# Kernel optimization log

Hardware: AMD Instinct MI355X
Metric: run time of the kernel (lower is better)

## Reference

```python
import jax, jax.numpy as jnp
import numpy as np

EPS_LN = 1e-5
EPS_ATTN = 1e-8
NUM_ITER = 3

B, N, DIN = 64, 4096, 256
K, D, H = 8, 256, 512


def layer_norm(x, g, b):
    m = jnp.mean(x, axis=-1, keepdims=True)
    v = jnp.mean((x - m) ** 2, axis=-1, keepdims=True)
    return (x - m) * jax.lax.rsqrt(v + EPS_LN) * g + b


def gru_cell(x, h, W_ih, b_ih, W_hh, b_hh):
    # torch GRUCell: gates ordered (reset, update, new)
    gi = x @ W_ih.T + b_ih  # [BK, 3D]
    gh = h @ W_hh.T + b_hh
    ir, iz, inn = jnp.split(gi, 3, axis=-1)
    hr, hz, hn = jnp.split(gh, 3, axis=-1)
    r = jax.nn.sigmoid(ir + hr)
    z = jax.nn.sigmoid(iz + hz)
    n = jnp.tanh(inn + r * hn)
    return (1.0 - z) * n + z * h


def setup_inputs() -> dict:
    key = jax.random.key(0)
    ks = jax.random.split(key, 16)
    s = 1.0 / np.sqrt(D)
    si = 1.0 / np.sqrt(DIN)
    inp = {
        'inputs': jax.random.normal(ks[0], (B, N, DIN), jnp.float32),
        'noise': jax.random.normal(ks[1], (B, K, D), jnp.float32),
        'slot_mu': jax.random.normal(ks[2], (1, 1, D), jnp.float32),
        'slot_log_sigma': jnp.zeros((1, 1, D), jnp.float32),
        'Wq': jax.random.uniform(ks[3], (D, D), jnp.float32, -s, s),
        'bq': jnp.zeros((D,), jnp.float32),
        'Wk': jax.random.uniform(ks[4], (D, DIN), jnp.float32, -si, si),
        'bk': jnp.zeros((D,), jnp.float32),
        'Wv': jax.random.uniform(ks[5], (D, DIN), jnp.float32, -si, si),
        'bv': jnp.zeros((D,), jnp.float32),
        'W_ih': jax.random.uniform(ks[6], (3 * D, D), jnp.float32, -s, s),
        'b_ih': jnp.zeros((3 * D,), jnp.float32),
        'W_hh': jax.random.uniform(ks[7], (3 * D, D), jnp.float32, -s, s),
        'b_hh': jnp.zeros((3 * D,), jnp.float32),
        'ln_in_g': jnp.ones((DIN,), jnp.float32), 'ln_in_b': jnp.zeros((DIN,), jnp.float32),
        'ln_s_g': jnp.ones((D,), jnp.float32), 'ln_s_b': jnp.zeros((D,), jnp.float32),
        'ln_ff_g': jnp.ones((D,), jnp.float32), 'ln_ff_b': jnp.zeros((D,), jnp.float32),
        'W1': jax.random.uniform(ks[8], (H, D), jnp.float32, -s, s),
        'b1': jnp.zeros((H,), jnp.float32),
        'W2': jax.random.uniform(ks[9], (D, H), jnp.float32, -1.0 / np.sqrt(H), 1.0 / np.sqrt(H)),
        'b2': jnp.zeros((D,), jnp.float32),
    }
    return inp


def reference(inputs, noise, slot_mu, slot_log_sigma, Wq, bq, Wk, bk, Wv, bv,
              W_ih, b_ih, W_hh, b_hh, ln_in_g, ln_in_b, ln_s_g, ln_s_b,
              ln_ff_g, ln_ff_b, W1, b1, W2, b2):
    scale = D ** -0.5
    slots = slot_mu + jnp.exp(slot_log_sigma) * noise  # [B,K,D]
    x = layer_norm(inputs, ln_in_g, ln_in_b)
    k = x @ Wk.T + bk  # [B,N,D]
    v = x @ Wv.T + bv  # [B,N,D]
    attn = None
    for _ in range(NUM_ITER):
        slots_prev = slots
        sn = layer_norm(slots, ln_s_g, ln_s_b)
        q = sn @ Wq.T + bq  # [B,K,D]
        dots = jnp.einsum('bkd,bnd->bkn', q, k) * scale
        attn = jax.nn.softmax(dots, axis=1)  # softmax over slots
        attn_norm = attn / (jnp.sum(attn, axis=-1, keepdims=True) + EPS_ATTN)
        updates = jnp.einsum('bkn,bnd->bkd', attn_norm, v)
        h = gru_cell(updates.reshape(-1, D), slots_prev.reshape(-1, D),
                     W_ih, b_ih, W_hh, b_hh).reshape(slots.shape)
        ff = layer_norm(h, ln_ff_g, ln_ff_b)
        slots = h + (jax.nn.relu(ff @ W1.T + b1) @ W2.T + b2)
    return slots, attn
```

## Files before the change

### kernel.cpp

```cpp
#include <hip/hip_runtime.h>
#include <hip/hip_bf16.h>
#include <math.h>

typedef __bf16 bf16x8 __attribute__((ext_vector_type(8)));
typedef float f32x4 __attribute__((ext_vector_type(4)));

#define DEV static __device__ __forceinline__

DEV unsigned short f2b(float f){
  unsigned int u = __float_as_uint(f);
  u += 0x7fffu + ((u>>16)&1u);
  return (unsigned short)(u>>16);
}
DEV float b2f(unsigned short h){ return __uint_as_float(((unsigned int)h)<<16); }
DEV unsigned int pck(float a, float b){
  return (unsigned int)f2b(a) | ((unsigned int)f2b(b)<<16);
}
DEV f32x4 mfma16(bf16x8 a, bf16x8 b, f32x4 c){
  return __builtin_amdgcn_mfma_f32_16x16x32_bf16(a,b,c,0,0,0);
}
DEV float sigm(float x){ return 1.f/(1.f+expf(-x)); }
#define RDLANE(v, l) __uint_as_float(__builtin_amdgcn_readlane(__float_as_uint(v), (l)))

__global__ __launch_bounds__(256) void k_slots_init(
    const float* __restrict__ noise, const float* __restrict__ mu,
    const float* __restrict__ ls, float* __restrict__ sf,
    unsigned short* __restrict__ sb){
  int i = blockIdx.x*256 + threadIdx.x;
  int d = i & 255;
  float val = mu[d] + expf(ls[d]) * noise[i];
  sf[i] = val; sb[i] = f2b(val);
}

__global__ __launch_bounds__(256) void k_prep_b16(
    const float* __restrict__ Whh, const float* __restrict__ W1,
    const float* __restrict__ W2,
    unsigned short* __restrict__ Whhb, unsigned short* __restrict__ W1b,
    unsigned short* __restrict__ W2b){
  int i = blockIdx.x*256 + threadIdx.x;
  if (i < 196608) Whhb[i] = f2b(Whh[i]);
  else if (i < 327680) W1b[i-196608] = f2b(W1[i-196608]);
  else if (i < 458752) W2b[i-327680] = f2b(W2[i-327680]);
}

__global__ __launch_bounds__(256) void k_pre1(
    const float* __restrict__ Wq, const float* __restrict__ Wk,
    const float* __restrict__ bq, const float* __restrict__ bk,
    unsigned short* __restrict__ WcT, float* __restrict__ bc,
    float* __restrict__ wqbk, float* __restrict__ cbk){
  int c = blockIdx.x, d = threadIdx.x;
  float acc = 0.f;
  for (int e=0;e<256;e++)
    acc += Wq[e*256+d] * Wk[e*256+c];
  WcT[c*256+d] = f2b(acc);
  __shared__ float red[256];
  red[d] = bq[d] * Wk[d*256+c];
  __syncthreads();
  for (int s2=128;s2>0;s2>>=1){ if (d<s2) red[d]+=red[d+s2]; __syncthreads(); }
  if (d==0) bc[c] = red[0];
  if (blockIdx.x==0){
    float a2=0.f;
    for (int e=0;e<256;e++) a2 += Wq[e*256+d]*bk[e];
    wqbk[d] = a2;
    __syncthreads();
    red[d] = bq[d]*bk[d];
    __syncthreads();
    for (int s2=128;s2>0;s2>>=1){ if (d<s2) red[d]+=red[d+s2]; __syncthreads(); }
    if (d==0) cbk[0] = red[0];
  }
}

__global__ __launch_bounds__(256) void k_pre2(
    const float* __restrict__ W_ih, const float* __restrict__ Wv,
    const float* __restrict__ bv, const float* __restrict__ b_ih,
    unsigned short* __restrict__ WvihT, float* __restrict__ bvih){
  int j = blockIdx.x, c = threadIdx.x;
  float acc=0.f;
  for (int d=0; d<256; d++)
    acc += W_ih[j*256+d] * Wv[d*256+c];
  WvihT[j*256+c] = f2b(acc);
  __shared__ float red[256];
  red[c] = bv[c] * W_ih[j*256+c];
  __syncthreads();
  for (int s2=128;s2>0;s2>>=1){ if (c<s2) red[c]+=red[c+s2]; __syncthreads(); }
  if (c==0) bvih[j] = red[0] + b_ih[j];
}

__global__ __launch_bounds__(256) void k_slot_q(
    const float* __restrict__ sf, const float* __restrict__ g,
    const float* __restrict__ be,
    const unsigned short* __restrict__ WcT, const float* __restrict__ bc,
    const float* __restrict__ wqbk, const float* __restrict__ cbk,
    unsigned short* __restrict__ qp, float* __restrict__ dotbias,
    float* __restrict__ attn_sum){
  __shared__ __align__(16) unsigned short sn[16][264];
  int b = blockIdx.x, t = threadIdx.x;
  if (t < 8) attn_sum[b*8+t] = 0.f;
  if (t < 8) dotbias[b*16+8+t] = 0.f;
  int r = t>>5, j = t&31;
  const float* pr = sf + (b*8+r)*256 + j*8;
  float v[8]; float s=0.f;
  #pragma unroll
  for (int i=0;i<8;i++){ v[i]=pr[i]; s+=v[i]; }
  s += __shfl_xor(s,1); s+=__shfl_xor(s,2); s+=__shfl_xor(s,4);
  s += __shfl_xor(s,8); s+=__shfl_xor(s,16);
  float m = s*(1.f/256.f);
  float vs=0.f;
  #pragma unroll
  for (int i=0;i<8;i++){ float d = v[i]-m; vs += d*d; }
  vs += __shfl_xor(vs,1); vs+=__shfl_xor(vs,2); vs+=__shfl_xor(vs,4);
  vs += __shfl_xor(vs,8); vs+=__shfl_xor(vs,16);
  float rstd = rsqrtf(vs*(1.f/256.f) + 1e-5f);
  float dp = 0.f;
  #pragma unroll
  for (int i=0;i<8;i++){
    int d = j*8+i;
    float snv = (v[i]-m)*rstd*g[d] + be[d];
    sn[r][d] = f2b(snv);
    dp += snv * wqbk[d];
  }
  dp += __shfl_xor(dp,1); dp+=__shfl_xor(dp,2); dp+=__shfl_xor(dp,4);
  dp += __shfl_xor(dp,8); dp+=__shfl_xor(dp,16);
  if (j==0) dotbias[b*16+r] = dp + cbk[0];
  for (int rr=8; rr<16; ++rr){ sn[rr][t]=0; if (t<8) sn[rr][256+t]=0; }
  __syncthreads();
  int lane = t&63, wv = t>>6, l16 = lane&15, quad = lane>>4;
  #pragma unroll
  for (int nt=0; nt<4; ++nt){
    int col = (wv*4+nt)*16 + l16;
    f32x4 acc = {0.f,0.f,0.f,0.f};
    #pragma unroll
    for (int kk=0;kk<8;kk++){
      int kd = kk*32 + quad*8;
      bf16x8 a = *(const bf16x8*)&sn[l16][kd];
      bf16x8 bb = *(const bf16x8*)(WcT + col*256 + kd);
      acc = mfma16(a,bb,acc);
    }
    float bcv = bc[col];
    #pragma unroll
    for (int ri=0;ri<4;ri++){
      int rw = quad*4+ri;
      qp[(b*16+rw)*256 + col] = f2b(acc[ri] + bcv);
    }
  }
}

__global__ __launch_bounds__(256) void k_iter0(
    const float* __restrict__ in, const float* __restrict__ g,
    const float* __restrict__ be, const unsigned short* __restrict__ qp,
    const float* __restrict__ dotbias, float* __restrict__ attn_sum,
    float* __restrict__ upart, unsigned short* __restrict__ xc_w){
  __shared__ __align__(16) unsigned short xt[64][264];
  int t = threadIdx.x;
  int b = blockIdx.x >> 4, sp = blockIdx.x & 15;
  int lane=t&63, wv=t>>6, l16=lane&15, quad=lane>>4;
  bf16x8 aq[8];
  #pragma unroll
  for (int kk=0;kk<8;kk++)
    aq[kk] = *(const bf16x8*)(qp + ((size_t)(b*16+l16))*256 + kk*32+quad*8);
  float db[4];
  #pragma unroll
  for (int ri=0;ri<4;ri++) db[ri] = dotbias[b*16 + quad*4 + ri];
  float acc[8][4];
  #pragma unroll
  for (int k2=0;k2<8;k2++){ acc[k2][0]=0;acc[k2][1]=0;acc[k2][2]=0;acc[k2][3]=0; }
  float rbs[4] = {0.f,0.f,0.f,0.f};
  int rl = t>>3, j = t&7;
  for (int tile=0; tile<4; ++tile){
    int n0 = sp*256 + tile*64;
    __syncthreads();
    #pragma unroll
    for (int p=0;p<2;p++){
      int row = p*32 + rl;
      const float* pr = in + ((size_t)(b*4096 + n0 + row))*256 + j*32;
      float v[32]; float s=0.f;
      #pragma unroll
      for (int c=0;c<8;c++) *(float4*)(v+c*4) = *(const float4*)(pr + c*4);
      #pragma unroll
      for (int i=0;i<32;i++) s += v[i];
      s += __shfl_xor(s,1); s+=__shfl_xor(s,2); s+=__shfl_xor(s,4);
      float m = s*(1.f/256.f);
      float vs=0.f;
      #pragma unroll
      for (int i=0;i<32;i++){ float d=v[i]-m; vs+=d*d; }
      vs+=__shfl_xor(vs,1); vs+=__shfl_xor(vs,2); vs+=__shfl_xor(vs,4);
      float rstd = rsqrtf(vs*(1.f/256.f)+1e-5f);
      #pragma unroll
      for (int c=0;c<4;c++){
        float o[8];
        #pragma unroll
        for (int q=0;q<8;q++){
          int d = j*32 + c*8 + q;
          o[q] = (v[c*8+q]-m)*rstd*g[d] + be[d];
        }
        uint4 w4;
        w4.x=pck(o[0],o[1]); w4.y=pck(o[2],o[3]);
        w4.z=pck(o[4],o[5]); w4.w=pck(o[6],o[7]);
        *(uint4*)&xt[row][j*32 + c*8] = w4;
        *(uint4*)(xc_w + ((size_t)(b*4096 + n0 + row))*256 + j*32 + c*8) = w4;
      }
    }
    __syncthreads();
    f32x4 dacc = {0.f,0.f,0.f,0.f};
    #pragma unroll
    for (int kk=0;kk<8;kk++){
      int kd = kk*32 + quad*8;
      bf16x8 bb = *(const bf16x8*)&xt[wv*16 + l16][kd];
      dacc = mfma16(aq[kk],bb,dacc);
    }
    const float scale = 0.0625f;
    float val[4];
    #pragma unroll
    for (int ri=0;ri<4;ri++) val[ri] = (dacc[ri] + db[ri]) * scale;
    float mx = fmaxf(fmaxf(val[0],val[1]), fmaxf(val[2],val[3]));
    mx = fmaxf(mx, __shfl_xor(mx,16));
    float e[4], s4=0.f;
    #pragma unroll
    for (int ri=0;ri<4;ri++){ e[ri] = expf(val[ri]-mx); s4 += e[ri]; }
    float s8 = s4 + __shfl_xor(s4,16);
    float inv = 1.f/s8;
    float av[4];
    #pragma unroll
    for (int ri=0;ri<4;ri++) av[ri] = e[ri]*inv;
    if (quad < 2){
      #pragma unroll
      for (int ri=0;ri<4;ri++){
        float ss = av[ri];
        ss += __shfl_xor(ss,1); ss+=__shfl_xor(ss,2);
        ss += __shfl_xor(ss,4); ss+=__shfl_xor(ss,8);
        if (l16==0) rbs[ri] += ss;
      }
    }
    #pragma unroll
    for (int nl=0; nl<16; ++nl){
      int n = wv*16 + nl;
      float xv0 = b2f(xt[n][lane]);
      float xv1 = b2f(xt[n][64+lane]);
      float xv2 = b2f(xt[n][128+lane]);
      float xv3 = b2f(xt[n][192+lane]);
      #pragma unroll
      for (int ri=0;ri<4;ri++){
        float alo = RDLANE(av[ri], nl);
        float ahi = RDLANE(av[ri], nl+16);
        acc[ri][0]   += alo*xv0; acc[ri][1]   += alo*xv1;
        acc[ri][2]   += alo*xv2; acc[ri][3]   += alo*xv3;
        acc[4+ri][0] += ahi*xv0; acc[4+ri][1] += ahi*xv1;
        acc[4+ri][2] += ahi*xv2; acc[4+ri][3] += ahi*xv3;
      }
    }
  }
  __syncthreads();
  float* ured = (float*)&xt[0][0];
  #pragma unroll
  for (int k2=0;k2<8;k2++)
    #pragma unroll
    for (int cc=0;cc<4;cc++)
      ured[(wv*8+k2)*256 + cc*64 + lane] = acc[k2][cc];
  __syncthreads();
  float* o = upart + (size_t)sp*131072 + ((size_t)b*8)*256 + t;
  #pragma unroll
  for (int k2=0;k2<8;k2++){
    float s = ured[k2*256+t] + ured[(8+k2)*256+t]
            + ured[(16+k2)*256+t] + ured[(24+k2)*256+t];
    o[(size_t)k2*256] = s;
  }
  if (quad < 2 && l16 == 0){
    #pragma unroll
    for (int ri=0;ri<4;ri++)
      atomicAdd(&attn_sum[b*8 + quad*4 + ri], rbs[ri]);
  }
}

__global__ __launch_bounds__(256) void k_iter(
    const unsigned short* __restrict__ xc,
    const unsigned short* __restrict__ qp,
    const float* __restrict__ dotbias, float* __restrict__ attn_sum,
    float* __restrict__ upart, float* __restrict__ attn_out){
  __shared__ __align__(16) unsigned short xt[64][264];
  int t = threadIdx.x;
  int b = blockIdx.x >> 4, sp = blockIdx.x & 15;
  int lane=t&63, wv=t>>6, l16=lane&15, quad=lane>>4;
  bf16x8 aq[8];
  #pragma unroll
  for (int kk=0;kk<8;kk++)
    aq[kk] = *(const bf16x8*)(qp + ((size_t)(b*16+l16))*256 + kk*32+quad*8);
  float db[4];
  #pragma unroll
  for (int ri=0;ri<4;ri++) db[ri] = dotbias[b*16 + quad*4 + ri];
  float acc[8][4];
  #pragma unroll
  for (int k2=0;k2<8;k2++){ acc[k2][0]=0;acc[k2][1]=0;acc[k2][2]=0;acc[k2][3]=0; }
  float rbs[4] = {0.f,0.f,0.f,0.f};
  int rl = t>>3, j = t&7;
  const unsigned short* cbase = xc + ((size_t)(b*4096 + sp*256))*256;
  uint4 R[8];
  #pragma unroll
  for (int p=0;p<2;p++){
    const unsigned short* pr = cbase + (size_t)(p*32+rl)*256 + j*32;
    #pragma unroll
    for (int c=0;c<4;c++) R[p*4+c] = *(const uint4*)(pr + c*8);
  }
  for (int tile=0; tile<4; ++tile){
    #pragma unroll
    for (int p=0;p<2;p++){
      #pragma unroll
      for (int c=0;c<4;c++)
        *(uint4*)&xt[p*32+rl][j*32 + c*8] = R[p*4+c];
    }
    __syncthreads();
    if (tile<3){
      const unsigned short* nb = cbase + (size_t)(tile+1)*64*256;
      #pragma unroll
      for (int p=0;p<2;p++){
        const unsigned short* pr = nb + (size_t)(p*32+rl)*256 + j*32;
        #pragma unroll
        for (int c=0;c<4;c++) R[p*4+c] = *(const uint4*)(pr + c*8);
      }
    }
    int n0 = sp*256 + tile*64;
    f32x4 dacc = {0.f,0.f,0.f,0.f};
    #pragma unroll
    for (int kk=0;kk<8;kk++){
      int kd = kk*32 + quad*8;
      bf16x8 bb = *(const bf16x8*)&xt[wv*16 + l16][kd];
      dacc = mfma16(aq[kk],bb,dacc);
    }
    const float scale = 0.0625f;
    float val[4];
    #pragma unroll
    for (int ri=0;ri<4;ri++) val[ri] = (dacc[ri] + db[ri]) * scale;
    float mx = fmaxf(fmaxf(val[0],val[1]), fmaxf(val[2],val[3]));
    mx = fmaxf(mx, __shfl_xor(mx,16));
    float e[4], s4=0.f;
    #pragma unroll
    for (int ri=0;ri<4;ri++){ e[ri] = expf(val[ri]-mx); s4 += e[ri]; }
    float s8 = s4 + __shfl_xor(s4,16);
    float inv = 1.f/s8;
    float av[4];
    #pragma unroll
    for (int ri=0;ri<4;ri++) av[ri] = e[ri]*inv;
    if (quad < 2){
      int nl = wv*16 + l16;
      #pragma unroll
      for (int ri=0;ri<4;ri++){
        int kr = quad*4+ri;
        if (attn_out)
          attn_out[((size_t)(b*8+kr))*4096 + n0 + nl] = av[ri];
        float ss = av[ri];
        ss += __shfl_xor(ss,1); ss+=__shfl_xor(ss,2);
        ss += __shfl_xor(ss,4); ss+=__shfl_xor(ss,8);
        if (l16==0) rbs[ri] += ss;
      }
    }
    #pragma unroll
    for (int nl=0; nl<16; ++nl){
      int n = wv*16 + nl;
      float xv0 = b2f(xt[n][lane]);
      float xv1 = b2f(xt[n][64+lane]);
      float xv2 = b2f(xt[n][128+lane]);
      float xv3 = b2f(xt[n][192+lane]);
      #pragma unroll
      for (int ri=0;ri<4;ri++){
        float alo = RDLANE(av[ri], nl);
        float ahi = RDLANE(av[ri], nl+16);
        acc[ri][0]   += alo*xv0; acc[ri][1]   += alo*xv1;
        acc[ri][2]   += alo*xv2; acc[ri][3]   += alo*xv3;
        acc[4+ri][0] += ahi*xv0; acc[4+ri][1] += ahi*xv1;
        acc[4+ri][2] += ahi*xv2; acc[4+ri][3] += ahi*xv3;
      }
    }
    __syncthreads();
  }
  float* ured = (float*)&xt[0][0];
  #pragma unroll
  for (int k2=0;k2<8;k2++)
    #pragma unroll
    for (int cc=0;cc<4;cc++)
      ured[(wv*8+k2)*256 + cc*64 + lane] = acc[k2][cc];
  __syncthreads();
  float* o = upart + (size_t)sp*131072 + ((size_t)b*8)*256 + t;
  #pragma unroll
  for (int k2=0;k2<8;k2++){
    float s = ured[k2*256+t] + ured[(8+k2)*256+t]
            + ured[(16+k2)*256+t] + ured[(24+k2)*256+t];
    o[(size_t)k2*256] = s;
  }
  if (quad < 2 && l16 == 0){
    #pragma unroll
    for (int ri=0;ri<4;ri++)
      atomicAdd(&attn_sum[b*8 + quad*4 + ri], rbs[ri]);
  }
}

__global__ __launch_bounds__(512) void k_step(
    const float* __restrict__ upart, float* __restrict__ asum,
    float* __restrict__ sf, unsigned short* __restrict__ sb,
    const unsigned short* __restrict__ WvihT, const float* __restrict__ bvih,
    const unsigned short* __restrict__ Whhb, const float* __restrict__ bhh,
    const float* __restrict__ lnffg, const float* __restrict__ lnffb,
    const unsigned short* __restrict__ W1b, const float* __restrict__ b1,
    const unsigned short* __restrict__ W2b, const float* __restrict__ b2v,
    const float* __restrict__ lnsg, const float* __restrict__ lnsb,
    const unsigned short* __restrict__ WcT, const float* __restrict__ bc,
    const float* __restrict__ wqbk, const float* __restrict__ cbk,
    unsigned short* __restrict__ qp, float* __restrict__ dotb,
    float* __restrict__ out_slots, int last){
  __shared__ __align__(16) unsigned short ub16[16][264];
  __shared__ __align__(16) float hls[16][268];
  __shared__ __align__(16) unsigned short sn[16][264];
  __shared__ __align__(16) unsigned short s1t[16][520];
  __shared__ float redh[8][16], redq[8][16], mr[16], rs[16];
  int t = threadIdx.x;
  int Bk = blockIdx.x;
  int bb0 = Bk*2;
  int lane=t&63, wv=t>>6, l16=lane&15, quad=lane>>4;
  {
    int r16 = t>>5, c0 = (t&31)*8;
    size_t base = ((size_t)(Bk*16 + r16))*256 + c0;
    float4 a0={0,0,0,0}, a1={0,0,0,0};
    #pragma unroll
    for (int sp2=0; sp2<16; ++sp2){
      const float* p = upart + (size_t)sp2*131072 + base;
      float4 u0=*(const float4*)(p+0), u1=*(const float4*)(p+4);
      a0.x+=u0.x;a0.y+=u0.y;a0.z+=u0.z;a0.w+=u0.w;
      a1.x+=u1.x;a1.y+=u1.y;a1.z+=u1.z;a1.w+=u1.w;
    }
    float inv = 1.f/(asum[Bk*16 + r16] + 1e-8f);
    float uu[8] = {a0.x,a0.y,a0.z,a0.w,a1.x,a1.y,a1.z,a1.w};
    #pragma unroll
    for (int c=0;c<8;c+=2)
      *(unsigned int*)&ub16[r16][c0+c] = pck(uu[c]*inv, uu[c+1]*inv);
  }
  __syncthreads();
  if (t < 16) asum[Bk*16 + t] = 0.f;
  bf16x8 afi[8], afh[8];
  #pragma unroll
  for (int kk=0;kk<8;kk++){
    int kd = kk*32+quad*8;
    afi[kk] = *(const bf16x8*)&ub16[l16][kd];
    afh[kk] = *(const bf16x8*)(sb + ((size_t)(Bk*16+l16))*256 + kd);
  }
  float sh[4]={0,0,0,0}, sq[4]={0,0,0,0};
  #pragma unroll
  for (int jj=0;jj<2;jj++){
    int jt = wv*2 + jj;
    int dR = jt*16 + l16;
    f32x4 cIR={0,0,0,0}, cIZ={0,0,0,0}, cIN={0,0,0,0};
    f32x4 cHR={0,0,0,0}, cHZ={0,0,0,0}, cHN={0,0,0,0};
    #pragma unroll
    for (int kk=0;kk<8;kk++){
      int kd = kk*32+quad*8;
      cIR = mfma16(afi[kk], *(const bf16x8*)(WvihT + (size_t)dR*256 + kd), cIR);
      cIZ = mfma16(afi[kk], *(const bf16x8*)(WvihT + (size_t)(256+dR)*256 + kd), cIZ);
      cIN = mfma16(afi[kk], *(const bf16x8*)(WvihT + (size_t)(512+dR)*256 + kd), cIN);
      cHR = mfma16(afh[kk], *(const bf16x8*)(Whhb + (size_t)dR*256 + kd), cHR);
      cHZ = mfma16(afh[kk], *(const bf16x8*)(Whhb + (size_t)(256+dR)*256 + kd), cHZ);
      cHN = mfma16(afh[kk], *(const bf16x8*)(Whhb + (size_t)(512+dR)*256 + kd), cHN);
    }
    float biR = bvih[dR], biZ = bvih[256+dR], biN = bvih[512+dR];
    float bhR = bhh[dR], bhZ = bhh[256+dR], bhN = bhh[512+dR];
    #pragma unroll
    for (int ri=0;ri<4;ri++){
      int row = quad*4+ri;
      float hp = sf[((size_t)(Bk*16+row))*256 + dR];
      float rg = sigm(cIR[ri]+biR + cHR[ri]+bhR);
      float z  = sigm(cIZ[ri]+biZ + cHZ[ri]+bhZ);
      float nn = tanhf(cIN[ri]+biN + rg*(cHN[ri]+bhN));
      float h = (1.f-z)*nn + z*hp;
      hls[row][dR] = h;
      sh[ri] += h; sq[ri] += h*h;
    }
  }
  #pragma unroll
  for (int ri=0;ri<4;ri++){
    sh[ri]+=__shfl_xor(sh[ri],1); sh[ri]+=__shfl_xor(sh[ri],2);
    sh[ri]+=__shfl_xor(sh[ri],4); sh[ri]+=__shfl_xor(sh[ri],8);
    sq[ri]+=__shfl_xor(sq[ri],1); sq[ri]+=__shfl_xor(sq[ri],2);
    sq[ri]+=__shfl_xor(sq[ri],4); sq[ri]+=__shfl_xor(sq[ri],8);
  }
  if (l16==0){
    #pragma unroll
    for (int ri=0;ri<4;ri++){
      redh[wv][quad*4+ri] = sh[ri];
      redq[wv][quad*4+ri] = sq[ri];
    }
  }
  __syncthreads();
  if (t < 16){
    float s = redh[0][t]+redh[1][t]+redh[2][t]+redh[3][t]
            + redh[4][t]+redh[5][t]+redh[6][t]+redh[7][t];
    float q = redq[0][t]+redq[1][t]+redq[2][t]+redq[3][t]
            + redq[4][t]+redq[5][t]+redq[6][t]+redq[7][t];
    float m = s*(1.f/256.f);
    float var = q*(1.f/256.f) - m*m;
    mr[t] = m; rs[t] = rsqrtf(var + 1e-5f);
  }
  __syncthreads();
  {
    int row = t>>5, c0 = (t&31)*8;
    float m = mr[row], rstd = rs[row];
    #pragma unroll
    for (int c=0;c<8;c+=2){
      int d = c0+c;
      float o0 = (hls[row][d]-m)*rstd*lnffg[d] + lnffb[d];
      float o1 = (hls[row][d+1]-m)*rstd*lnffg[d+1] + lnffb[d+1];
      *(unsigned int*)&sn[row][d] = pck(o0,o1);
    }
  }
  __syncthreads();
  {
    bf16x8 af[8];
    #pragma unroll
    for (int kk=0;kk<8;kk++)
      af[kk] = *(const bf16x8*)&sn[l16][kk*32+quad*8];
    #pragma unroll
    for (int ct=wv*4; ct<wv*4+4; ++ct){
      int col = ct*16+l16;
      f32x4 acc={0,0,0,0};
      #pragma unroll
      for (int kk=0;kk<8;kk++)
        acc = mfma16(af[kk], *(const bf16x8*)(W1b + (size_t)col*256 + kk*32+quad*8), acc);
      float bb = b1[col];
      #pragma unroll
      for (int ri=0;ri<4;ri++){
        float v2 = acc[ri]+bb; v2 = v2>0.f? v2:0.f;
        s1t[quad*4+ri][col] = f2b(v2);
      }
    }
  }
  __syncthreads();
  {
    bf16x8 af[16];
    #pragma unroll
    for (int kk=0;kk<16;kk++)
      af[kk] = *(const bf16x8*)&s1t[l16][kk*32+quad*8];
    #pragma unroll
    for (int ct=wv*2; ct<wv*2+2; ++ct){
      int col = ct*16+l16;
      f32x4 acc={0,0,0,0};
      #pragma unroll
      for (int kk=0;kk<16;kk++)
        acc = mfma16(af[kk], *(const bf16x8*)(W2b + (size_t)col*512 + kk*32+quad*8), acc);
      float bb = b2v[col];
      #pragma unroll
      for (int ri=0;ri<4;ri++){
        int row = quad*4+ri;
        float v2 = acc[ri] + bb + hls[row][col];
        size_t gidx = ((size_t)(Bk*16+row))*256 + col;
        sf[gidx] = v2;
        sb[gidx] = f2b(v2);
        if (last) out_slots[gidx] = v2;
        hls[row][col] = v2;
      }
    }
  }
  if (!last){
    __syncthreads();
    {
      int row = t>>5, c0 = (t&31)*8;
      float ps=0.f, pq=0.f;
      float hv[8];
      #pragma unroll
      for (int c=0;c<8;c++){ hv[c]=hls[row][c0+c]; ps+=hv[c]; pq+=hv[c]*hv[c]; }
      ps+=__shfl_xor(ps,1); ps+=__shfl_xor(ps,2); ps+=__shfl_xor(ps,4);
      ps+=__shfl_xor(ps,8); ps+=__shfl_xor(ps,16);
      pq+=__shfl_xor(pq,1); pq+=__shfl_xor(pq,2); pq+=__shfl_xor(pq,4);
      pq+=__shfl_xor(pq,8); pq+=__shfl_xor(pq,16);
      float m = ps*(1.f/256.f);
      float var = pq*(1.f/256.f) - m*m;
      float rstd = rsqrtf(var + 1e-5f);
      float dp = 0.f;
      #pragma unroll
      for (int c=0;c<8;c+=2){
        int d = c0+c;
        float o0 = (hv[c]-m)*rstd*lnsg[d] + lnsb[d];
        float o1 = (hv[c+1]-m)*rstd*lnsg[d+1] + lnsb[d+1];
        dp += o0*wqbk[d] + o1*wqbk[d+1];
        *(unsigned int*)&sn[row][d] = pck(o0,o1);
      }
      dp+=__shfl_xor(dp,1); dp+=__shfl_xor(dp,2); dp+=__shfl_xor(dp,4);
      dp+=__shfl_xor(dp,8); dp+=__shfl_xor(dp,16);
      if ((t&31)==0){
        int bloc = row>>3, rr = row&7;
        dotb[(bb0+bloc)*16 + rr] = dp + cbk[0];
      }
    }
    __syncthreads();
    {
      bf16x8 af[8];
      #pragma unroll
      for (int kk=0;kk<8;kk++)
        af[kk] = *(const bf16x8*)&sn[l16][kk*32+quad*8];
      #pragma unroll
      for (int ct=wv*2; ct<wv*2+2; ++ct){
        int col = ct*16+l16;
        f32x4 acc={0,0,0,0};
        #pragma unroll
        for (int kk=0;kk<8;kk++)
          acc = mfma16(af[kk], *(const bf16x8*)(WcT + (size_t)col*256 + kk*32+quad*8), acc);
        float bcv = bc[col];
        #pragma unroll
        for (int ri=0;ri<4;ri++){
          int row = quad*4+ri;
          int bloc = row>>3, rr = row&7;
          qp[((size_t)((bb0+bloc)*16 + rr))*256 + col] = f2b(acc[ri] + bcv);
        }
      }
    }
  }
}

extern "C" void kernel_launch(void* const* d_in, const int* in_sizes, int n_in,
                              void* d_out, int out_size, void* d_ws, size_t ws_size,
                              hipStream_t stream){
  const float* inputs  = (const float*)d_in[0];
  const float* noise   = (const float*)d_in[1];
  const float* slot_mu = (const float*)d_in[2];
  const float* slot_ls = (const float*)d_in[3];
  const float* Wq   = (const float*)d_in[4];
  const float* bq   = (const float*)d_in[5];
  const float* Wk   = (const float*)d_in[6];
  const float* bk   = (const float*)d_in[7];
  const float* Wv   = (const float*)d_in[8];
  const float* bv   = (const float*)d_in[9];
  const float* W_ih = (const float*)d_in[10];
  const float* b_ih = (const float*)d_in[11];
  const float* W_hh = (const float*)d_in[12];
  const float* b_hh = (const float*)d_in[13];
  const float* ln_in_g = (const float*)d_in[14];
  const float* ln_in_b = (const float*)d_in[15];
  const float* ln_s_g  = (const float*)d_in[16];
  const float* ln_s_b  = (const float*)d_in[17];
  const float* ln_ff_g = (const float*)d_in[18];
  const float* ln_ff_b = (const float*)d_in[19];
  const float* W1 = (const float*)d_in[20];
  const float* b1 = (const float*)d_in[21];
  const float* W2 = (const float*)d_in[22];
  const float* b2 = (const float*)d_in[23];

  char* w = (char*)d_ws;
  auto alloc = [&](size_t n)->char*{ char* p=w; w += (n+255)&~(size_t)255; return p; };
  unsigned short* xc   = (unsigned short*)alloc(134217728);
  float* upart         = (float*)alloc(8388608);
  unsigned short* qp   = (unsigned short*)alloc(524288);
  float* sf            = (float*)alloc(524288);
  unsigned short* sb   = (unsigned short*)alloc(262144);
  unsigned short* WcT  = (unsigned short*)alloc(131072);
  unsigned short* WvihT= (unsigned short*)alloc(393216);
  unsigned short* Whhb = (unsigned short*)alloc(393216);
  unsigned short* W1b  = (unsigned short*)alloc(262144);
  unsigned short* W2b  = (unsigned short*)alloc(262144);
  float* bc    = (float*)alloc(1024);
  float* wqbk  = (float*)alloc(1024);
  float* cbk   = (float*)alloc(256);
  float* bvih  = (float*)alloc(3072);
  float* dotb  = (float*)alloc(4096);
  float* asum  = (float*)alloc(2048);

  float* out_slots = (float*)d_out;
  float* out_attn  = out_slots + 131072;

  k_slots_init<<<dim3(512),dim3(256),0,stream>>>(noise, slot_mu, slot_ls, sf, sb);
  k_pre1<<<dim3(256),dim3(256),0,stream>>>(Wq, Wk, bq, bk, WcT, bc, wqbk, cbk);
  k_pre2<<<dim3(768),dim3(256),0,stream>>>(W_ih, Wv, bv, b_ih, WvihT, bvih);
  k_prep_b16<<<dim3(1792),dim3(256),0,stream>>>(W_hh, W1, W2, Whhb, W1b, W2b);
  k_slot_q<<<dim3(64),dim3(256),0,stream>>>(sf, ln_s_g, ln_s_b, WcT, bc, wqbk, cbk,
                                            qp, dotb, asum);

  for (int it=0; it<3; ++it){
    int last = (it==2);
    if (it==0){
      k_iter0<<<dim3(1024),dim3(256),0,stream>>>(
          inputs, ln_in_g, ln_in_b, qp, dotb, asum, upart, xc);
    } else {
      k_iter<<<dim3(1024),dim3(256),0,stream>>>(
          xc, qp, dotb, asum, upart,
          last ? out_attn : (float*)nullptr);
    }
    k_step<<<dim3(32),dim3(512),0,stream>>>(
        upart, asum, sf, sb, WvihT, bvih, Whhb, b_hh,
        ln_ff_g, ln_ff_b, W1b, b1, W2b, b2,
        ln_s_g, ln_s_b, WcT, bc, wqbk, cbk,
        qp, dotb, last ? out_slots : (float*)nullptr, last);
  }
}
```

Baseline: 855.5 us.

## Compute attention-weighted value sums with MFMA using hi/lo bf16 split

Replaces the scalar FMA plus readlane accumulation of attn×x with MFMA, treating the attention weights as a 16-row A matrix (8 high bf16 rows plus 8 low residual rows) stored in shared memory. The x tile moves to a blocked shared layout so the transposed B operand can be gathered, and the cross-wave reduction through LDS is dropped because each wave now owns its own output columns. It also removes the register prefetch of the next x tile in k_iter, making those loads synchronous, and adds an extra barrier per tile. Gathering B with scalar 16-bit LDS reads may offset part of the gain.

Result: faster. 717.9 us (-16.1%).

```diff
diff --git a/kernel.cpp b/kernel.cpp
--- a/kernel.cpp
+++ b/kernel.cpp
@@ -20,7 +20,11 @@
   return __builtin_amdgcn_mfma_f32_16x16x32_bf16(a,b,c,0,0,0);
 }
 DEV float sigm(float x){ return 1.f/(1.f+expf(-x)); }
-#define RDLANE(v, l) __uint_as_float(__builtin_amdgcn_readlane(__float_as_uint(v), (l)))
+
+DEV int xti(int n, int d){
+  return (n>>2)*1160 + (d>>4)*72 + (n&3)*16 + (d&15);
+}
+#define XT_ELEMS 18560
 
 __global__ __launch_bounds__(256) void k_slots_init(
     const float* __restrict__ noise, const float* __restrict__ mu,
@@ -145,12 +149,14 @@
   }
 }
 
+
 __global__ __launch_bounds__(256) void k_iter0(
     const float* __restrict__ in, const float* __restrict__ g,
     const float* __restrict__ be, const unsigned short* __restrict__ qp,
     const float* __restrict__ dotbias, float* __restrict__ attn_sum,
     float* __restrict__ upart, unsigned short* __restrict__ xc_w){
-  __shared__ __align__(16) unsigned short xt[64][264];
+  __shared__ __align__(16) unsigned short xt[XT_ELEMS];
+  __shared__ __align__(16) unsigned short PTm[16][72];
   int t = threadIdx.x;
   int b = blockIdx.x >> 4, sp = blockIdx.x & 15;
   int lane=t&63, wv=t>>6, l16=lane&15, quad=lane>>4;
@@ -161,51 +167,50 @@
   float db[4];
   #pragma unroll
   for (int ri=0;ri<4;ri++) db[ri] = dotbias[b*16 + quad*4 + ri];
-  float acc[8][4];
-  #pragma unroll
-  for (int k2=0;k2<8;k2++){ acc[k2][0]=0;acc[k2][1]=0;acc[k2][2]=0;acc[k2][3]=0; }
+  f32x4 acc4[4];
+  #pragma unroll
+  for (int i=0;i<4;i++){ acc4[i][0]=0;acc4[i][1]=0;acc4[i][2]=0;acc4[i][3]=0; }
   float rbs[4] = {0.f,0.f,0.f,0.f};
-  int rl = t>>3, j = t&7;
+  int rl2 = t>>4, j2 = t&15;
   for (int tile=0; tile<4; ++tile){
     int n0 = sp*256 + tile*64;
     __syncthreads();
     #pragma unroll
-    for (int p=0;p<2;p++){
-      int row = p*32 + rl;
-      const float* pr = in + ((size_t)(b*4096 + n0 + row))*256 + j*32;
-      float v[32]; float s=0.f;
-      #pragma unroll
-      for (int c=0;c<8;c++) *(float4*)(v+c*4) = *(const float4*)(pr + c*4);
-      #pragma unroll
-      for (int i=0;i<32;i++) s += v[i];
-      s += __shfl_xor(s,1); s+=__shfl_xor(s,2); s+=__shfl_xor(s,4);
+    for (int p=0;p<4;p++){
+      int row = p*16 + rl2;
+      const float* pr = in + ((size_t)(b*4096 + n0 + row))*256 + j2*16;
+      float v[16]; float s=0.f;
+      #pragma unroll
+      for (int c=0;c<4;c++) *(float4*)(v+c*4) = *(const float4*)(pr + c*4);
+      #pragma unroll
+      for (int i=0;i<16;i++) s += v[i];
+      s += __shfl_xor(s,1); s+=__shfl_xor(s,2); s+=__shfl_xor(s,4); s+=__shfl_xor(s,8);
       float m = s*(1.f/256.f);
       float vs=0.f;
       #pragma unroll
-      for (int i=0;i<32;i++){ float d=v[i]-m; vs+=d*d; }
-      vs+=__shfl_xor(vs,1); vs+=__shfl_xor(vs,2); vs+=__shfl_xor(vs,4);
+      for (int i=0;i<16;i++){ float d=v[i]-m; vs+=d*d; }
+      vs+=__shfl_xor(vs,1); vs+=__shfl_xor(vs,2); vs+=__shfl_xor(vs,4); vs+=__shfl_xor(vs,8);
       float rstd = rsqrtf(vs*(1.f/256.f)+1e-5f);
       #pragma unroll
-      for (int c=0;c<4;c++){
+      for (int c=0;c<2;c++){
         float o[8];
         #pragma unroll
         for (int q=0;q<8;q++){
-          int d = j*32 + c*8 + q;
+          int d = j2*16 + c*8 + q;
           o[q] = (v[c*8+q]-m)*rstd*g[d] + be[d];
         }
         uint4 w4;
         w4.x=pck(o[0],o[1]); w4.y=pck(o[2],o[3]);
         w4.z=pck(o[4],o[5]); w4.w=pck(o[6],o[7]);
-        *(uint4*)&xt[row][j*32 + c*8] = w4;
-        *(uint4*)(xc_w + ((size_t)(b*4096 + n0 + row))*256 + j*32 + c*8) = w4;
+        *(uint4*)&xt[xti(row, j2*16 + c*8)] = w4;
+        *(uint4*)(xc_w + ((size_t)(b*4096 + n0 + row))*256 + j2*16 + c*8) = w4;
       }
     }
     __syncthreads();
     f32x4 dacc = {0.f,0.f,0.f,0.f};
     #pragma unroll
     for (int kk=0;kk<8;kk++){
-      int kd = kk*32 + quad*8;
-      bf16x8 bb = *(const bf16x8*)&xt[wv*16 + l16][kd];
+      bf16x8 bb = *(const bf16x8*)&xt[xti(wv*16 + l16, kk*32 + quad*8)];
       dacc = mfma16(aq[kk],bb,dacc);
     }
     const float scale = 0.0625f;
@@ -223,46 +228,50 @@
     #pragma unroll
     for (int ri=0;ri<4;ri++) av[ri] = e[ri]*inv;
     if (quad < 2){
+      int nn = wv*16 + l16;
       #pragma unroll
       for (int ri=0;ri<4;ri++){
+        unsigned short h = f2b(av[ri]);
+        unsigned short lw = f2b(av[ri] - b2f(h));
+        PTm[quad*4+ri][nn] = h;
+        PTm[8+quad*4+ri][nn] = lw;
         float ss = av[ri];
         ss += __shfl_xor(ss,1); ss+=__shfl_xor(ss,2);
         ss += __shfl_xor(ss,4); ss+=__shfl_xor(ss,8);
         if (l16==0) rbs[ri] += ss;
       }
     }
-    #pragma unroll
-    for (int nl=0; nl<16; ++nl){
-      int n = wv*16 + nl;
-      float xv0 = b2f(xt[n][lane]);
-      float xv1 = b2f(xt[n][64+lane]);
-      float xv2 = b2f(xt[n][128+lane]);
-      float xv3 = b2f(xt[n][192+lane]);
-      #pragma unroll
-      for (int ri=0;ri<4;ri++){
-        float alo = RDLANE(av[ri], nl);
-        float ahi = RDLANE(av[ri], nl+16);
-        acc[ri][0]   += alo*xv0; acc[ri][1]   += alo*xv1;
-        acc[ri][2]   += alo*xv2; acc[ri][3]   += alo*xv3;
-        acc[4+ri][0] += ahi*xv0; acc[4+ri][1] += ahi*xv1;
-        acc[4+ri][2] += ahi*xv2; acc[4+ri][3] += ahi*xv3;
-      }
-    }
-  }
-  __syncthreads();
-  float* ured = (float*)&xt[0][0];
-  #pragma unroll
-  for (int k2=0;k2<8;k2++)
-    #pragma unroll
-    for (int cc=0;cc<4;cc++)
-      ured[(wv*8+k2)*256 + cc*64 + lane] = acc[k2][cc];
-  __syncthreads();
-  float* o = upart + (size_t)sp*131072 + ((size_t)b*8)*256 + t;
-  #pragma unroll
-  for (int k2=0;k2<8;k2++){
-    float s = ured[k2*256+t] + ured[(8+k2)*256+t]
-            + ured[(16+k2)*256+t] + ured[(24+k2)*256+t];
-    o[(size_t)k2*256] = s;
+    __syncthreads();
+    bf16x8 pa0 = *(const bf16x8*)&PTm[l16][quad*8];
+    bf16x8 pa1 = *(const bf16x8*)&PTm[l16][32 + quad*8];
+    #pragma unroll
+    for (int i=0;i<4;i++){
+      int cOff = (wv*4+i)*72 + l16;
+      #pragma unroll
+      for (int kk2=0;kk2<2;kk2++){
+        int base = (kk2*8 + quad*2)*1160 + cOff;
+        unsigned short xv[8];
+        #pragma unroll
+        for (int j=0;j<8;j++)
+          xv[j] = xt[base + (j&3)*16 + (j>>2)*1160];
+        union { unsigned u[4]; bf16x8 v; } U;
+        #pragma unroll
+        for (int w2=0;w2<4;w2++)
+          U.u[w2] = (unsigned)xv[2*w2] | ((unsigned)xv[2*w2+1]<<16);
+        acc4[i] = mfma16(kk2 ? pa1 : pa0, U.v, acc4[i]);
+      }
+    }
+  }
+  float* o = upart + (size_t)sp*131072 + ((size_t)b*8)*256;
+  #pragma unroll
+  for (int i=0;i<4;i++){
+    #pragma unroll
+    for (int ri=0;ri<4;ri++){
+      float hiv = acc4[i][ri];
+      float lov = __shfl_xor(hiv, 32);
+      if (quad < 2)
+        o[(quad*4+ri)*256 + (wv*4+i)*16 + l16] = hiv + lov;
+    }
   }
   if (quad < 2 && l16 == 0){
     #pragma unroll
@@ -276,7 +285,8 @@
     const unsigned short* __restrict__ qp,
     const float* __restrict__ dotbias, float* __restrict__ attn_sum,
     float* __restrict__ upart, float* __restrict__ attn_out){
-  __shared__ __align__(16) unsigned short xt[64][264];
+  __shared__ __align__(16) unsigned short xt[XT_ELEMS];
+  __shared__ __align__(16) unsigned short PTm[16][72];
   int t = threadIdx.x;
   int b = blockIdx.x >> 4, sp = blockIdx.x & 15;
   int lane=t&63, wv=t>>6, l16=lane&15, quad=lane>>4;
@@ -287,42 +297,30 @@
   float db[4];
   #pragma unroll
   for (int ri=0;ri<4;ri++) db[ri] = dotbias[b*16 + quad*4 + ri];
-  float acc[8][4];
-  #pragma unroll
-  for (int k2=0;k2<8;k2++){ acc[k2][0]=0;acc[k2][1]=0;acc[k2][2]=0;acc[k2][3]=0; }
+  f32x4 acc4[4];
+  #pragma unroll
+  for (int i=0;i<4;i++){ acc4[i][0]=0;acc4[i][1]=0;acc4[i][2]=0;acc4[i][3]=0; }
   float rbs[4] = {0.f,0.f,0.f,0.f};
   int rl = t>>3, j = t&7;
   const unsigned short* cbase = xc + ((size_t)(b*4096 + sp*256))*256;
-  uint4 R[8];
-  #pragma unroll
-  for (int p=0;p<2;p++){
-    const unsigned short* pr = cbase + (size_t)(p*32+rl)*256 + j*32;
-    #pragma unroll
-    for (int c=0;c<4;c++) R[p*4+c] = *(const uint4*)(pr + c*8);
-  }
   for (int tile=0; tile<4; ++tile){
+    __syncthreads();
+    const unsigned short* tb = cbase + (size_t)tile*64*256;
     #pragma unroll
     for (int p=0;p<2;p++){
-      #pragma unroll
-      for (int c=0;c<4;c++)
-        *(uint4*)&xt[p*32+rl][j*32 + c*8] = R[p*4+c];
-    }
-    __syncthreads();
-    if (tile<3){
-      const unsigned short* nb = cbase + (size_t)(tile+1)*64*256;
-      #pragma unroll
-      for (int p=0;p<2;p++){
-        const unsigned short* pr = nb + (size_t)(p*32+rl)*256 + j*32;
-        #pragma unroll
-        for (int c=0;c<4;c++) R[p*4+c] = *(const uint4*)(pr + c*8);
-      }
-    }
-    int n0 = sp*256 + tile*64;
+      int row = p*32 + rl;
+      const unsigned short* pr = tb + (size_t)row*256 + j*32;
+      #pragma unroll
+      for (int c=0;c<4;c++){
+        uint4 w4 = *(const uint4*)(pr + c*8);
+        *(uint4*)&xt[xti(row, j*32 + c*8)] = w4;
+      }
+    }
+    __syncthreads();
     f32x4 dacc = {0.f,0.f,0.f,0.f};
     #pragma unroll
     for (int kk=0;kk<8;kk++){
-      int kd = kk*32 + quad*8;
-      bf16x8 bb = *(const bf16x8*)&xt[wv*16 + l16][kd];
+      bf16x8 bb = *(const bf16x8*)&xt[xti(wv*16 + l16, kk*32 + quad*8)];
       dacc = mfma16(aq[kk],bb,dacc);
     }
     const float scale = 0.0625f;
@@ -339,51 +337,55 @@
     float av[4];
     #pragma unroll
     for (int ri=0;ri<4;ri++) av[ri] = e[ri]*inv;
+    int n0 = sp*256 + tile*64;
     if (quad < 2){
-      int nl = wv*16 + l16;
+      int nn = wv*16 + l16;
       #pragma unroll
       for (int ri=0;ri<4;ri++){
         int kr = quad*4+ri;
+        unsigned short h = f2b(av[ri]);
+        unsigned short lw = f2b(av[ri] - b2f(h));
+        PTm[kr][nn] = h;
+        PTm[8+kr][nn] = lw;
         if (attn_out)
-          attn_out[((size_t)(b*8+kr))*4096 + n0 + nl] = av[ri];
+          attn_out[((size_t)(b*8+kr))*4096 + n0 + nn] = av[ri];
         float ss = av[ri];
         ss += __shfl_xor(ss,1); ss+=__shfl_xor(ss,2);
         ss += __shfl_xor(ss,4); ss+=__shfl_xor(ss,8);
         if (l16==0) rbs[ri] += ss;
       }
     }
-    #pragma unroll
-    for (int nl=0; nl<16; ++nl){
-      int n = wv*16 + nl;
-      float xv0 = b2f(xt[n][lane]);
-      float xv1 = b2f(xt[n][64+lane]);
-      float xv2 = b2f(xt[n][128+lane]);
-      float xv3 = b2f(xt[n][192+lane]);
-      #pragma unroll
-      for (int ri=0;ri<4;ri++){
-        float alo = RDLANE(av[ri], nl);
-        float ahi = RDLANE(av[ri], nl+16);
-        acc[ri][0]   += alo*xv0; acc[ri][1]   += alo*xv1;
-        acc[ri][2]   += alo*xv2; acc[ri][3]   += alo*xv3;
-        acc[4+ri][0] += ahi*xv0; acc[4+ri][1] += ahi*xv1;
-        acc[4+ri][2] += ahi*xv2; acc[4+ri][3] += ahi*xv3;
-      }
-    }
-    __syncthreads();
-  }
-  float* ured = (float*)&xt[0][0];
-  #pragma unroll
-  for (int k2=0;k2<8;k2++)
-    #pragma unroll
-    for (int cc=0;cc<4;cc++)
-      ured[(wv*8+k2)*256 + cc*64 + lane] = acc[k2][cc];
-  __syncthreads();
-  float* o = upart + (size_t)sp*131072 + ((size_t)b*8)*256 + t;
-  #pragma unroll
-  for (int k2=0;k2<8;k2++){
-    float s = ured[k2*256+t] + ured[(8+k2)*256+t]
-            + ured[(16+k2)*256+t] + ured[(24+k2)*256+t];
-    o[(size_t)k2*256] = s;
+    __syncthreads();
+    bf16x8 pa0 = *(const bf16x8*)&PTm[l16][quad*8];
+    bf16x8 pa1 = *(const bf16x8*)&PTm[l16][32 + quad*8];
+    #pragma unroll
+    for (int i=0;i<4;i++){
+      int cOff = (wv*4+i)*72 + l16;
+      #pragma unroll
+      for (int kk2=0;kk2<2;kk2++){
+        int base = (kk2*8 + quad*2)*1160 + cOff;
+        unsigned short xv[8];
+        #pragma unroll
+        for (int jj=0;jj<8;jj++)
+          xv[jj] = xt[base + (jj&3)*16 + (jj>>2)*1160];
+        union { unsigned u[4]; bf16x8 v; } U;
+        #pragma unroll
+        for (int w2=0;w2<4;w2++)
+          U.u[w2] = (unsigned)xv[2*w2] | ((unsigned)xv[2*w2+1]<<16);
+        acc4[i] = mfma16(kk2 ? pa1 : pa0, U.v, acc4[i]);
+      }
+    }
+  }
+  float* o = upart + (size_t)sp*131072 + ((size_t)b*8)*256;
+  #pragma unroll
+  for (int i=0;i<4;i++){
+    #pragma unroll
+    for (int ri=0;ri<4;ri++){
+      float hiv = acc4[i][ri];
+      float lov = __shfl_xor(hiv, 32);
+      if (quad < 2)
+        o[(quad*4+ri)*256 + (wv*4+i)*16 + l16] = hiv + lov;
+    }
   }
   if (quad < 2 && l16 == 0){
     #pragma unroll
```
